# Optimization experiments

Measured on AMD Instinct MI355X. Metric: run time of the kernel, lower is better.

Reference implementation:

```python
import jax, jax.numpy as jnp
import numpy as np

N = 50000
IN_DIM = 512
HID = 64
E = 800000


def setup_inputs() -> dict:
    key = jax.random.key(0)
    k1, k2, k3, k4 = jax.random.split(key, 4)
    x = jax.random.normal(k1, (N, IN_DIM), dtype=jnp.float32)
    edge_index = jax.random.randint(k2, (2, E), 0, N, dtype=jnp.int32)
    # Glorot-ish init for linear weights
    W1 = jax.random.normal(k3, (IN_DIM, HID), dtype=jnp.float32) / np.sqrt(IN_DIM)
    b1 = jnp.zeros((HID,), dtype=jnp.float32)
    W2 = jax.random.normal(k4, (HID, HID), dtype=jnp.float32) / np.sqrt(HID)
    b2 = jnp.zeros((HID,), dtype=jnp.float32)
    return {"x": x, "edge_index": edge_index, "W1": W1, "b1": b1, "W2": W2, "b2": b2}


def gcn_conv(x, src, dst, norm, W, b, n):
    # x' = D^{-1/2} (A+I) D^{-1/2} x W + b  (PyG GCNConv with self-loops)
    h = x @ W                                  # [N, out] dense GEMM
    msg = h[src] * norm[:, None]               # gather + scale per edge
    out = jax.ops.segment_sum(msg, dst, num_segments=n)  # scatter-add
    return out + b


def reference(x, edge_index, W1, b1, W2, b2):
    n = x.shape[0]
    loop = jnp.arange(n, dtype=edge_index.dtype)
    src = jnp.concatenate([edge_index[0], loop])  # add self-loops
    dst = jnp.concatenate([edge_index[1], loop])
    deg = jax.ops.segment_sum(jnp.ones_like(src, dtype=x.dtype), dst, num_segments=n)
    dinv = jnp.where(deg > 0, jax.lax.rsqrt(deg), 0.0)
    norm = dinv[src] * dinv[dst]               # symmetric normalization per edge
    h = gcn_conv(x, src, dst, norm, W1, b1, n)
    h = jax.nn.relu(h)
    # dropout is identity in eval mode (reference baseline)
    z = gcn_conv(h, src, dst, norm, W2, b2, n)
    return z
```

## Files before the change

kernel.cpp:

```cpp
#include <hip/hip_runtime.h>
#include <stdint.h>


typedef __attribute__((ext_vector_type(8))) short short8;
typedef __attribute__((ext_vector_type(4))) float f32x4;
typedef __attribute__((ext_vector_type(4))) unsigned int u32x4;

#define SLOTS 64

__device__ __forceinline__ uint32_t bf16_rne(float f) {
  uint32_t u = __float_as_uint(f);
  return (u + 0x7FFFu + ((u >> 16) & 1u)) >> 16;
}

__device__ __forceinline__ uint32_t cvt_pk_bf16(float a, float b) {
  uint32_t r;
  asm("v_cvt_pk_bf16_f32 %0, %1, %2" : "=v"(r) : "v"(a), "v"(b));
  return r;
}

__global__ __launch_bounds__(256) void fill_wfrag_kernel(
    const int* __restrict__ src, const int* __restrict__ dst, int E,
    int* __restrict__ cursor, int* __restrict__ meta,
    const float* __restrict__ W1, const float* __restrict__ W2,
    short8* __restrict__ wh1, short8* __restrict__ wl1,
    short8* __restrict__ wh2, short8* __restrict__ wl2,
    int K1, int K2, int wblocks) {
  if ((int)blockIdx.x >= wblocks) {
    int i = (blockIdx.x - wblocks) * 256 + threadIdx.x;
    if (i < E) {
      int s = __builtin_nontemporal_load(src + i);
      int d = __builtin_nontemporal_load(dst + i);
      int pos = atomicAdd(&cursor[d], 1);
      if (pos < SLOTS) meta[(size_t)d * SLOTS + pos] = s;
    }
    return;
  }
  int idx = blockIdx.x * 256 + threadIdx.x;
  int tot1 = (K1 >> 5) * 256;
  int tot2 = (K2 >> 5) * 256;
  const float* W;
  short8 *wh, *wl;
  if (idx < tot1) {
    W = W1; wh = wh1; wl = wl1;
  } else if (idx < tot1 + tot2) {
    idx -= tot1;
    W = W2; wh = wh2; wl = wl2;
  } else {
    return;
  }
  int lane = idx & 63;
  int ct = (idx >> 6) & 3;
  int kt = idx >> 8;
  int m = lane & 15, q = lane >> 4;
  int col = ct * 16 + m;
  short8 h, l;
#pragma unroll
  for (int j = 0; j < 8; ++j) {
    float f = W[(size_t)(kt * 32 + q * 8 + j) * 64 + col];
    uint32_t hb = bf16_rne(f);
    float hf = __uint_as_float(hb << 16);
    float lo = f - hf;
    h[j] = (short)hb;
    l[j] = (short)bf16_rne(lo);
  }
  wh[idx] = h;
  wl[idx] = l;
}

__global__ __launch_bounds__(256) void gemm_mfma_kernel(
    const float* __restrict__ A, const short8* __restrict__ wh,
    const short8* __restrict__ wl, const int* __restrict__ deg,
    ushort* __restrict__ outb, int n, int K) {
  const int t = threadIdx.x;
  const int lane = t & 63;
  const int m = lane & 15, q = lane >> 4;
  const int row0 = blockIdx.x * 128 + (t >> 6) * 32;
  int r0 = row0 + m;
  int r1 = row0 + 16 + m;
  if (r0 >= n) r0 = n - 1;
  if (r1 >= n) r1 = n - 1;
  const float* ap0 = A + (size_t)r0 * K + q * 8;
  const float* ap1 = A + (size_t)r1 * K + q * 8;
  const short8* whp = wh + lane;
  const short8* wlp = wl + lane;
  const int nkt = K >> 5;
  f32x4 acc[2][4];
#pragma unroll
  for (int g = 0; g < 2; ++g)
#pragma unroll
    for (int c = 0; c < 4; ++c) acc[g][c] = 0.f;

  f32x4 xa0 = *(const f32x4*)(ap0);
  f32x4 xa1 = *(const f32x4*)(ap0 + 4);
  f32x4 xb0 = *(const f32x4*)(ap1);
  f32x4 xb1 = *(const f32x4*)(ap1 + 4);
  short8 bh[4] = {whp[0], whp[64], whp[128], whp[192]};
  short8 bl[4] = {wlp[0], wlp[64], wlp[128], wlp[192]};

  auto cvt = [&](const f32x4& u0, const f32x4& u1, short8& hi, short8& lo) {
    u32x4 hw, lw;
    hw[0] = cvt_pk_bf16(u0[0], u0[1]);
    hw[1] = cvt_pk_bf16(u0[2], u0[3]);
    hw[2] = cvt_pk_bf16(u1[0], u1[1]);
    hw[3] = cvt_pk_bf16(u1[2], u1[3]);
    lw[0] = cvt_pk_bf16(u0[0] - __uint_as_float(hw[0] << 16),
                        u0[1] - __uint_as_float(hw[0] & 0xFFFF0000u));
    lw[1] = cvt_pk_bf16(u0[2] - __uint_as_float(hw[1] << 16),
                        u0[3] - __uint_as_float(hw[1] & 0xFFFF0000u));
    lw[2] = cvt_pk_bf16(u1[0] - __uint_as_float(hw[2] << 16),
                        u1[1] - __uint_as_float(hw[2] & 0xFFFF0000u));
    lw[3] = cvt_pk_bf16(u1[2] - __uint_as_float(hw[3] << 16),
                        u1[3] - __uint_as_float(hw[3] & 0xFFFF0000u));
    hi = __builtin_bit_cast(short8, hw);
    lo = __builtin_bit_cast(short8, lw);
  };
  auto compute = [&]() {
    short8 ah0, al0, ah1, al1;
    cvt(xa0, xa1, ah0, al0);
    cvt(xb0, xb1, ah1, al1);
#pragma unroll
    for (int c = 0; c < 4; ++c) {
      acc[0][c] = __builtin_amdgcn_mfma_f32_16x16x32_bf16(ah0, bh[c], acc[0][c], 0, 0, 0);
      acc[1][c] = __builtin_amdgcn_mfma_f32_16x16x32_bf16(ah1, bh[c], acc[1][c], 0, 0, 0);
    }
#pragma unroll
    for (int c = 0; c < 4; ++c) {
      acc[0][c] = __builtin_amdgcn_mfma_f32_16x16x32_bf16(ah0, bl[c], acc[0][c], 0, 0, 0);
      acc[1][c] = __builtin_amdgcn_mfma_f32_16x16x32_bf16(ah1, bl[c], acc[1][c], 0, 0, 0);
    }
#pragma unroll
    for (int c = 0; c < 4; ++c) {
      acc[0][c] = __builtin_amdgcn_mfma_f32_16x16x32_bf16(al0, bh[c], acc[0][c], 0, 0, 0);
      acc[1][c] = __builtin_amdgcn_mfma_f32_16x16x32_bf16(al1, bh[c], acc[1][c], 0, 0, 0);
    }
  };

  for (int kt = 0; kt < nkt - 1; ++kt) {
    const float* an0 = ap0 + 32;
    const float* an1 = ap1 + 32;
    f32x4 nxa0 = *(const f32x4*)(an0);
    f32x4 nxa1 = *(const f32x4*)(an0 + 4);
    f32x4 nxb0 = *(const f32x4*)(an1);
    f32x4 nxb1 = *(const f32x4*)(an1 + 4);
    const short8* whn = whp + 256;
    const short8* wln = wlp + 256;
    short8 nh[4] = {whn[0], whn[64], whn[128], whn[192]};
    short8 nl[4] = {wln[0], wln[64], wln[128], wln[192]};
    compute();
    xa0 = nxa0; xa1 = nxa1; xb0 = nxb0; xb1 = nxb1;
#pragma unroll
    for (int c = 0; c < 4; ++c) { bh[c] = nh[c]; bl[c] = nl[c]; }
    ap0 = an0; ap1 = an1; whp = whn; wlp = wln;
  }
  compute();

#pragma unroll
  for (int g = 0; g < 2; ++g)
#pragma unroll
    for (int i = 0; i < 4; ++i) {
      int rr = row0 + g * 16 + q * 4 + i;
      if (rr < n) {
        float s = rsqrtf((float)(deg[rr] + 1));
        ushort* op = outb + (size_t)rr * 64 + m;
        op[0]  = (ushort)bf16_rne(acc[g][0][i] * s);
        op[16] = (ushort)bf16_rne(acc[g][1][i] * s);
        op[32] = (ushort)bf16_rne(acc[g][2][i] * s);
        op[48] = (ushort)bf16_rne(acc[g][3][i] * s);
      }
    }
}

__global__ __launch_bounds__(256) void agg_kernel(const ushort* __restrict__ H,
                                                  const int* __restrict__ deg,
                                                  const int* __restrict__ meta,
                                                  const float* __restrict__ bias,
                                                  float* __restrict__ out, int n,
                                                  int do_relu) {
  const int t = threadIdx.x;
  const int sl = t & 7;
  const int v = blockIdx.x * 32 + (t >> 3);
  if (v >= n) return;
  int dg = deg[v];
  const float dv = rsqrtf((float)(dg + 1));
  float acc[8];
  {
    uint4 hv = *(const uint4*)&H[(size_t)v * 64 + (sl << 3)];
    uint32_t u[4] = {hv.x, hv.y, hv.z, hv.w};
#pragma unroll
    for (int j = 0; j < 4; ++j) {
      acc[2 * j]     = __uint_as_float(u[j] << 16);
      acc[2 * j + 1] = __uint_as_float(u[j] & 0xFFFF0000u);
    }
  }
  if (dg > SLOTS) dg = SLOTS;
  int nc = (dg + 7) >> 3;
  const int4* p = (const int4*)(meta + (size_t)v * SLOTS);

  int4 ma0, ma1, mb0, mb1;
  uint4 ra[8], rb[8];
  auto gath = [&](int4 c0, int4 c1, uint4* r) {
    int u[8] = {c0.x, c0.y, c0.z, c0.w, c1.x, c1.y, c1.z, c1.w};
#pragma unroll
    for (int j = 0; j < 8; ++j) {
      unsigned idx = (unsigned)u[j];
      if (idx >= (unsigned)n) idx = 0;
      r[j] = *(const uint4*)&H[(size_t)idx * 64 + (sl << 3)];
    }
  };
  auto consume = [&](int rem, const uint4* r) {
#pragma unroll
    for (int j = 0; j < 8; ++j) {
      const float wgt = (j < rem) ? 1.f : 0.f;
      uint32_t q[4] = {r[j].x, r[j].y, r[j].z, r[j].w};
#pragma unroll
      for (int k = 0; k < 4; ++k) {
        acc[2 * k]     = fmaf(__uint_as_float(q[k] << 16), wgt, acc[2 * k]);
        acc[2 * k + 1] = fmaf(__uint_as_float(q[k] & 0xFFFF0000u), wgt, acc[2 * k + 1]);
      }
    }
  };

  if (nc > 0) {
    ma0 = p[0]; ma1 = p[1];
    gath(ma0, ma1, ra);
  }
  for (int c = 0; c < nc - 1; ++c) {
    mb0 = p[2 * c + 2]; mb1 = p[2 * c + 3];
    gath(mb0, mb1, rb);
    consume(dg - (c << 3), ra);
    ma0 = mb0; ma1 = mb1;
#pragma unroll
    for (int j = 0; j < 8; ++j) ra[j] = rb[j];
  }
  if (nc > 0) consume(dg - ((nc - 1) << 3), ra);

  const float4 blo = *(const float4*)&bias[sl << 3];
  const float4 bhi = *(const float4*)&bias[(sl << 3) + 4];
  float bb[8] = {blo.x, blo.y, blo.z, blo.w, bhi.x, bhi.y, bhi.z, bhi.w};
#pragma unroll
  for (int j = 0; j < 8; ++j) {
    acc[j] = fmaf(acc[j], dv, bb[j]);
    if (do_relu) acc[j] = fmaxf(acc[j], 0.f);
  }
  float* op = out + (size_t)v * 64 + (sl << 3);
  f32x4 v0 = {acc[0], acc[1], acc[2], acc[3]};
  f32x4 v1 = {acc[4], acc[5], acc[6], acc[7]};
  if (do_relu) {
    *(f32x4*)op = v0;
    *(f32x4*)(op + 4) = v1;
  } else {
    __builtin_nontemporal_store(v0, (f32x4*)op);
    __builtin_nontemporal_store(v1, (f32x4*)(op + 4));
  }
}

extern "C" void kernel_launch(void* const* d_in, const int* in_sizes, int n_in,
                              void* d_out, int out_size, void* d_ws, size_t ws_size,
                              hipStream_t stream) {
  const float* x = (const float*)d_in[0];
  const int* ei = (const int*)d_in[1];
  const float* W1 = (const float*)d_in[2];
  const float* b1 = (const float*)d_in[3];
  const float* W2 = (const float*)d_in[4];
  const float* b2 = (const float*)d_in[5];
  float* out = (float*)d_out;

  const int HID = in_sizes[3];
  const int IN_DIM = in_sizes[2] / HID;
  const int N = in_sizes[0] / IN_DIM;
  const int E = in_sizes[1] / 2;

  uint8_t* p = (uint8_t*)d_ws;
  auto alloc = [&](size_t bytes) {
    void* r = (void*)p;
    p += (bytes + 255) & ~(size_t)255;
    return r;
  };
  int* meta = (int*)alloc((size_t)N * SLOTS * 4);
  int* cursor = (int*)alloc((size_t)N * 4);
  ushort* hb = (ushort*)alloc((size_t)N * HID * 2);
  float* h = (float*)alloc((size_t)N * HID * 4);
  short8* wh1 = (short8*)alloc((size_t)(IN_DIM >> 5) * 256 * 16);
  short8* wl1 = (short8*)alloc((size_t)(IN_DIM >> 5) * 256 * 16);
  short8* wh2 = (short8*)alloc((size_t)(HID >> 5) * 256 * 16);
  short8* wl2 = (short8*)alloc((size_t)(HID >> 5) * 256 * 16);

  const int* srcp = ei;
  const int* dstp = ei + E;

  (void)hipMemsetAsync(cursor, 0, (size_t)N * 4, stream);

  const int wtot = (IN_DIM >> 5) * 256 + (HID >> 5) * 256;
  const int wblocks = (wtot + 255) / 256;
  const int fblocks = (E + 255) / 256;
  fill_wfrag_kernel<<<wblocks + fblocks, 256, 0, stream>>>(
      srcp, dstp, E, cursor, meta, W1, W2, wh1, wl1, wh2, wl2, IN_DIM, HID, wblocks);

  const int g1 = (N + 127) / 128;
  gemm_mfma_kernel<<<g1, 256, 0, stream>>>(x, wh1, wl1, cursor, hb, N, IN_DIM);
  agg_kernel<<<(N + 31) / 32, 256, 0, stream>>>(hb, cursor, meta, b1, h, N, 1);
  gemm_mfma_kernel<<<g1, 256, 0, stream>>>(h, wh2, wl2, cursor, hb, N, HID);
  agg_kernel<<<(N + 31) / 32, 256, 0, stream>>>(hb, cursor, meta, b2, out, N, 0);
}
```

Before: 265.9 us.

## Split aggregation into two column-half passes with nontemporal index loads

Each aggregation kernel now handles only 32 of the 64 feature columns, using 4 threads per node instead of 8, and is launched twice with a column offset. The aim is to halve the gathered bf16 row footprint per pass so that the working set of H stays resident in cache during the random gathers. The edge index (meta) loads become nontemporal so they do not evict H lines, and the layer-1 output store also becomes nontemporal. The cost is reading the neighbour lists and degrees twice and adding an extra launch per layer.

```diff
diff --git a/kernel.cpp b/kernel.cpp
--- a/kernel.cpp
+++ b/kernel.cpp
@@ -5,6 +5,7 @@
 typedef __attribute__((ext_vector_type(8))) short short8;
 typedef __attribute__((ext_vector_type(4))) float f32x4;
 typedef __attribute__((ext_vector_type(4))) unsigned int u32x4;
+typedef __attribute__((ext_vector_type(4))) int i32x4;
 
 #define SLOTS 64
 
@@ -176,16 +177,17 @@
                                                   const int* __restrict__ meta,
                                                   const float* __restrict__ bias,
                                                   float* __restrict__ out, int n,
-                                                  int do_relu) {
+                                                  int do_relu, int colofs) {
   const int t = threadIdx.x;
-  const int sl = t & 7;
-  const int v = blockIdx.x * 32 + (t >> 3);
+  const int sl = t & 3;
+  const int v = blockIdx.x * 64 + (t >> 2);
   if (v >= n) return;
+  const int cb = colofs + (sl << 3);
   int dg = deg[v];
   const float dv = rsqrtf((float)(dg + 1));
   float acc[8];
   {
-    uint4 hv = *(const uint4*)&H[(size_t)v * 64 + (sl << 3)];
+    uint4 hv = *(const uint4*)&H[(size_t)v * 64 + cb];
     uint32_t u[4] = {hv.x, hv.y, hv.z, hv.w};
 #pragma unroll
     for (int j = 0; j < 4; ++j) {
@@ -195,17 +197,17 @@
   }
   if (dg > SLOTS) dg = SLOTS;
   int nc = (dg + 7) >> 3;
-  const int4* p = (const int4*)(meta + (size_t)v * SLOTS);
-
-  int4 ma0, ma1, mb0, mb1;
+  const i32x4* p = (const i32x4*)(meta + (size_t)v * SLOTS);
+
+  i32x4 ma0, ma1, mb0, mb1;
   uint4 ra[8], rb[8];
-  auto gath = [&](int4 c0, int4 c1, uint4* r) {
-    int u[8] = {c0.x, c0.y, c0.z, c0.w, c1.x, c1.y, c1.z, c1.w};
+  auto gath = [&](const i32x4& c0, const i32x4& c1, uint4* r) {
+    int u[8] = {c0[0], c0[1], c0[2], c0[3], c1[0], c1[1], c1[2], c1[3]};
 #pragma unroll
     for (int j = 0; j < 8; ++j) {
       unsigned idx = (unsigned)u[j];
       if (idx >= (unsigned)n) idx = 0;
-      r[j] = *(const uint4*)&H[(size_t)idx * 64 + (sl << 3)];
+      r[j] = *(const uint4*)&H[(size_t)idx * 64 + cb];
     }
   };
   auto consume = [&](int rem, const uint4* r) {
@@ -222,11 +224,13 @@
   };
 
   if (nc > 0) {
-    ma0 = p[0]; ma1 = p[1];
+    ma0 = __builtin_nontemporal_load(p + 0);
+    ma1 = __builtin_nontemporal_load(p + 1);
     gath(ma0, ma1, ra);
   }
   for (int c = 0; c < nc - 1; ++c) {
-    mb0 = p[2 * c + 2]; mb1 = p[2 * c + 3];
+    mb0 = __builtin_nontemporal_load(p + 2 * c + 2);
+    mb1 = __builtin_nontemporal_load(p + 2 * c + 3);
     gath(mb0, mb1, rb);
     consume(dg - (c << 3), ra);
     ma0 = mb0; ma1 = mb1;
@@ -235,24 +239,19 @@
   }
   if (nc > 0) consume(dg - ((nc - 1) << 3), ra);
 
-  const float4 blo = *(const float4*)&bias[sl << 3];
-  const float4 bhi = *(const float4*)&bias[(sl << 3) + 4];
+  const float4 blo = *(const float4*)&bias[cb];
+  const float4 bhi = *(const float4*)&bias[cb + 4];
   float bb[8] = {blo.x, blo.y, blo.z, blo.w, bhi.x, bhi.y, bhi.z, bhi.w};
 #pragma unroll
   for (int j = 0; j < 8; ++j) {
     acc[j] = fmaf(acc[j], dv, bb[j]);
     if (do_relu) acc[j] = fmaxf(acc[j], 0.f);
   }
-  float* op = out + (size_t)v * 64 + (sl << 3);
+  float* op = out + (size_t)v * 64 + cb;
   f32x4 v0 = {acc[0], acc[1], acc[2], acc[3]};
   f32x4 v1 = {acc[4], acc[5], acc[6], acc[7]};
-  if (do_relu) {
-    *(f32x4*)op = v0;
-    *(f32x4*)(op + 4) = v1;
-  } else {
-    __builtin_nontemporal_store(v0, (f32x4*)op);
-    __builtin_nontemporal_store(v1, (f32x4*)(op + 4));
-  }
+  __builtin_nontemporal_store(v0, (f32x4*)op);
+  __builtin_nontemporal_store(v1, (f32x4*)(op + 4));
 }
 
 extern "C" void kernel_launch(void* const* d_in, const int* in_sizes, int n_in,
@@ -298,8 +297,11 @@
       srcp, dstp, E, cursor, meta, W1, W2, wh1, wl1, wh2, wl2, IN_DIM, HID, wblocks);
 
   const int g1 = (N + 127) / 128;
+  const int ga = (N + 63) / 64;
   gemm_mfma_kernel<<<g1, 256, 0, stream>>>(x, wh1, wl1, cursor, hb, N, IN_DIM);
-  agg_kernel<<<(N + 31) / 32, 256, 0, stream>>>(hb, cursor, meta, b1, h, N, 1);
+  agg_kernel<<<ga, 256, 0, stream>>>(hb, cursor, meta, b1, h, N, 1, 0);
+  agg_kernel<<<ga, 256, 0, stream>>>(hb, cursor, meta, b1, h, N, 1, 32);
   gemm_mfma_kernel<<<g1, 256, 0, stream>>>(h, wh2, wl2, cursor, hb, N, HID);
-  agg_kernel<<<(N + 31) / 32, 256, 0, stream>>>(hb, cursor, meta, b2, out, N, 0);
-}
+  agg_kernel<<<ga, 256, 0, stream>>>(hb, cursor, meta, b2, out, N, 0, 0);
+  agg_kernel<<<ga, 256, 0, stream>>>(hb, cursor, meta, b2, out, N, 0, 32);
+}
```

Measured after the change: 295.7 us. 1.11x slower.

## Overlap edge bucketing with first GEMM by moving source scaling into aggregation

Applied to the files above, without the earlier changes.

The edge-bucketing pass moves out of the weight-fragment kernel and into the first GEMM launch as extra leading blocks. The GEMM can no longer read finished degrees, so the per-source D^-1/2 scaling moves into the aggregation kernel: each gathered neighbour's weight becomes rsqrt(deg+1), read from the cursor array. The memset is replaced by a zeroing path in the weight-fragment kernel. This removes a serial dependency and one launch, at the cost of an extra scattered 4-byte degree load per edge in both aggregation passes.

```diff
diff --git a/kernel.cpp b/kernel.cpp
--- a/kernel.cpp
+++ b/kernel.cpp
@@ -19,21 +19,14 @@
   return r;
 }
 
-__global__ __launch_bounds__(256) void fill_wfrag_kernel(
-    const int* __restrict__ src, const int* __restrict__ dst, int E,
-    int* __restrict__ cursor, int* __restrict__ meta,
+__global__ __launch_bounds__(256) void wfrag_zero_kernel(
     const float* __restrict__ W1, const float* __restrict__ W2,
     short8* __restrict__ wh1, short8* __restrict__ wl1,
     short8* __restrict__ wh2, short8* __restrict__ wl2,
-    int K1, int K2, int wblocks) {
+    int K1, int K2, int wblocks, int* __restrict__ cursor, int n) {
   if ((int)blockIdx.x >= wblocks) {
     int i = (blockIdx.x - wblocks) * 256 + threadIdx.x;
-    if (i < E) {
-      int s = __builtin_nontemporal_load(src + i);
-      int d = __builtin_nontemporal_load(dst + i);
-      int pos = atomicAdd(&cursor[d], 1);
-      if (pos < SLOTS) meta[(size_t)d * SLOTS + pos] = s;
-    }
+    if (i < n) cursor[i] = 0;
     return;
   }
   int idx = blockIdx.x * 256 + threadIdx.x;
@@ -68,14 +61,26 @@
   wl[idx] = l;
 }
 
-__global__ __launch_bounds__(256) void gemm_mfma_kernel(
+__global__ __launch_bounds__(256) void gemm_fill_kernel(
     const float* __restrict__ A, const short8* __restrict__ wh,
-    const short8* __restrict__ wl, const int* __restrict__ deg,
-    ushort* __restrict__ outb, int n, int K) {
+    const short8* __restrict__ wl, ushort* __restrict__ outb, int n, int K,
+    int fblocks, const int* __restrict__ src, const int* __restrict__ dst, int E,
+    int* __restrict__ cursor, int* __restrict__ meta) {
+  if ((int)blockIdx.x < fblocks) {
+    int i = blockIdx.x * 256 + threadIdx.x;
+    if (i < E) {
+      int s = __builtin_nontemporal_load(src + i);
+      int d = __builtin_nontemporal_load(dst + i);
+      int pos = atomicAdd(&cursor[d], 1);
+      if (pos < SLOTS) meta[(size_t)d * SLOTS + pos] = s;
+    }
+    return;
+  }
+  const int bid = blockIdx.x - fblocks;
   const int t = threadIdx.x;
   const int lane = t & 63;
   const int m = lane & 15, q = lane >> 4;
-  const int row0 = blockIdx.x * 128 + (t >> 6) * 32;
+  const int row0 = bid * 128 + (t >> 6) * 32;
   int r0 = row0 + m;
   int r1 = row0 + 16 + m;
   if (r0 >= n) r0 = n - 1;
@@ -161,18 +166,17 @@
     for (int i = 0; i < 4; ++i) {
       int rr = row0 + g * 16 + q * 4 + i;
       if (rr < n) {
-        float s = rsqrtf((float)(deg[rr] + 1));
         ushort* op = outb + (size_t)rr * 64 + m;
-        op[0]  = (ushort)bf16_rne(acc[g][0][i] * s);
-        op[16] = (ushort)bf16_rne(acc[g][1][i] * s);
-        op[32] = (ushort)bf16_rne(acc[g][2][i] * s);
-        op[48] = (ushort)bf16_rne(acc[g][3][i] * s);
+        op[0]  = (ushort)bf16_rne(acc[g][0][i]);
+        op[16] = (ushort)bf16_rne(acc[g][1][i]);
+        op[32] = (ushort)bf16_rne(acc[g][2][i]);
+        op[48] = (ushort)bf16_rne(acc[g][3][i]);
       }
     }
 }
 
 __global__ __launch_bounds__(256) void agg_kernel(const ushort* __restrict__ H,
-                                                  const int* __restrict__ deg,
+                                                  const int* __restrict__ cursor,
                                                   const int* __restrict__ meta,
                                                   const float* __restrict__ bias,
                                                   float* __restrict__ out, int n,
@@ -181,37 +185,39 @@
   const int sl = t & 7;
   const int v = blockIdx.x * 32 + (t >> 3);
   if (v >= n) return;
-  int dg = deg[v];
-  const float dv = rsqrtf((float)(dg + 1));
+  const int dgc = cursor[v];
+  const float dv = rsqrtf((float)(dgc + 1));
   float acc[8];
   {
     uint4 hv = *(const uint4*)&H[(size_t)v * 64 + (sl << 3)];
     uint32_t u[4] = {hv.x, hv.y, hv.z, hv.w};
 #pragma unroll
     for (int j = 0; j < 4; ++j) {
-      acc[2 * j]     = __uint_as_float(u[j] << 16);
-      acc[2 * j + 1] = __uint_as_float(u[j] & 0xFFFF0000u);
-    }
-  }
-  if (dg > SLOTS) dg = SLOTS;
+      acc[2 * j]     = __uint_as_float(u[j] << 16) * dv;
+      acc[2 * j + 1] = __uint_as_float(u[j] & 0xFFFF0000u) * dv;
+    }
+  }
+  int dg = dgc > SLOTS ? SLOTS : dgc;
   int nc = (dg + 7) >> 3;
   const int4* p = (const int4*)(meta + (size_t)v * SLOTS);
 
   int4 ma0, ma1, mb0, mb1;
   uint4 ra[8], rb[8];
-  auto gath = [&](int4 c0, int4 c1, uint4* r) {
+  int ca[8], cb[8];
+  auto gath = [&](int4 c0, int4 c1, uint4* r, int* cw) {
     int u[8] = {c0.x, c0.y, c0.z, c0.w, c1.x, c1.y, c1.z, c1.w};
 #pragma unroll
     for (int j = 0; j < 8; ++j) {
       unsigned idx = (unsigned)u[j];
       if (idx >= (unsigned)n) idx = 0;
       r[j] = *(const uint4*)&H[(size_t)idx * 64 + (sl << 3)];
-    }
-  };
-  auto consume = [&](int rem, const uint4* r) {
+      cw[j] = cursor[idx];
+    }
+  };
+  auto consume = [&](int rem, const uint4* r, const int* cw) {
 #pragma unroll
     for (int j = 0; j < 8; ++j) {
-      const float wgt = (j < rem) ? 1.f : 0.f;
+      const float wgt = (j < rem) ? rsqrtf((float)(cw[j] + 1)) : 0.f;
       uint32_t q[4] = {r[j].x, r[j].y, r[j].z, r[j].w};
 #pragma unroll
       for (int k = 0; k < 4; ++k) {
@@ -223,17 +229,17 @@
 
   if (nc > 0) {
     ma0 = p[0]; ma1 = p[1];
-    gath(ma0, ma1, ra);
+    gath(ma0, ma1, ra, ca);
   }
   for (int c = 0; c < nc - 1; ++c) {
     mb0 = p[2 * c + 2]; mb1 = p[2 * c + 3];
-    gath(mb0, mb1, rb);
-    consume(dg - (c << 3), ra);
+    gath(mb0, mb1, rb, cb);
+    consume(dg - (c << 3), ra, ca);
     ma0 = mb0; ma1 = mb1;
 #pragma unroll
-    for (int j = 0; j < 8; ++j) ra[j] = rb[j];
-  }
-  if (nc > 0) consume(dg - ((nc - 1) << 3), ra);
+    for (int j = 0; j < 8; ++j) { ra[j] = rb[j]; ca[j] = cb[j]; }
+  }
+  if (nc > 0) consume(dg - ((nc - 1) << 3), ra, ca);
 
   const float4 blo = *(const float4*)&bias[sl << 3];
   const float4 bhi = *(const float4*)&bias[(sl << 3) + 4];
@@ -289,17 +295,18 @@
   const int* srcp = ei;
   const int* dstp = ei + E;
 
-  (void)hipMemsetAsync(cursor, 0, (size_t)N * 4, stream);
-
   const int wtot = (IN_DIM >> 5) * 256 + (HID >> 5) * 256;
   const int wblocks = (wtot + 255) / 256;
+  const int zblocks = (N + 255) / 256;
+  wfrag_zero_kernel<<<wblocks + zblocks, 256, 0, stream>>>(
+      W1, W2, wh1, wl1, wh2, wl2, IN_DIM, HID, wblocks, cursor, N);
+
   const int fblocks = (E + 255) / 256;
-  fill_wfrag_kernel<<<wblocks + fblocks, 256, 0, stream>>>(
-      srcp, dstp, E, cursor, meta, W1, W2, wh1, wl1, wh2, wl2, IN_DIM, HID, wblocks);
-
   const int g1 = (N + 127) / 128;
-  gemm_mfma_kernel<<<g1, 256, 0, stream>>>(x, wh1, wl1, cursor, hb, N, IN_DIM);
+  gemm_fill_kernel<<<fblocks + g1, 256, 0, stream>>>(
+      x, wh1, wl1, hb, N, IN_DIM, fblocks, srcp, dstp, E, cursor, meta);
   agg_kernel<<<(N + 31) / 32, 256, 0, stream>>>(hb, cursor, meta, b1, h, N, 1);
-  gemm_mfma_kernel<<<g1, 256, 0, stream>>>(h, wh2, wl2, cursor, hb, N, HID);
+  gemm_fill_kernel<<<g1, 256, 0, stream>>>(
+      h, wh2, wl2, hb, N, HID, 0, nullptr, nullptr, 0, nullptr, nullptr);
   agg_kernel<<<(N + 31) / 32, 256, 0, stream>>>(hb, cursor, meta, b2, out, N, 0);
 }
```

Result: slower. 281.8 us (+6.0%).
